# Performance work log

Measured on AMD Instinct MI355X. Metric: run time of the kernel, lower is better.

The kernel has to match this reference:

```python
import jax, jax.numpy as jnp
import numpy as np

HEADS = 16

def setup_inputs() -> dict:
    key = jax.random.key(0)
    ks = jax.random.split(key, 8)
    N, S, E = 4, 2048, 1024
    D = E // HEADS
    values = jax.random.normal(ks[0], (N, S, E), jnp.float32)
    keys_t = jax.random.normal(ks[1], (N, S, E), jnp.float32)
    query = jax.random.normal(ks[2], (N, S, E), jnp.float32)
    mask = jnp.ones((N, 1, 1, S), jnp.float32)  # broadcasts vs (N,H,Q,K)
    # keras Dense(head_dim, use_bias=False) on last-dim head_dim input: kernel (D, D)
    Wv = jax.random.normal(ks[3], (D, D), jnp.float32) * 0.05
    Wk = jax.random.normal(ks[4], (D, D), jnp.float32) * 0.05
    Wq = jax.random.normal(ks[5], (D, D), jnp.float32) * 0.05
    Wo = jax.random.normal(ks[6], (E, E), jnp.float32) * 0.02
    bo = jnp.zeros((E,), jnp.float32)
    return {"values": values, "keys": keys_t, "query": query, "mask": mask,
            "Wv": Wv, "Wk": Wk, "Wq": Wq, "Wo": Wo, "bo": bo}

def reference(values, keys, query, mask, Wv, Wk, Wq, Wo, bo):
    N, S, E = values.shape
    H = HEADS
    D = E // H
    # reshape to (N, len, H, D), then per-head shared Dense(D) projections
    v = values.reshape(N, S, H, D) @ Wv
    k = keys.reshape(N, S, H, D) @ Wk
    q = query.reshape(N, query.shape[1], H, D) @ Wq
    energy = jnp.einsum('nqhd,nkhd->nhqk', q, k)  # (N,H,Q,K)
    energy = jnp.where(mask == 0, jnp.float32(-1e20), energy)
    # NOTE: scaled by sqrt(embed_size), matching the original module
    attn = jax.nn.softmax(energy / jnp.sqrt(jnp.float32(E)), axis=3)
    out = jnp.einsum('nhql,nlhd->nqhd', attn, v)  # (N,Q,H,D)
    out = out.reshape(N, q.shape[1], E)
    return out @ Wo + bo
```

## Files before the change

### kernel.cpp

```cpp
#include <hip/hip_runtime.h>


typedef unsigned short u16;
typedef __attribute__((ext_vector_type(8))) short s16x8;
typedef __attribute__((ext_vector_type(8))) unsigned short u16x8;
typedef __attribute__((ext_vector_type(4))) float f32x4;
typedef __attribute__((ext_vector_type(4))) unsigned int u32x4;

#define GLL16(gsrc, ldst)                                                     \
    __builtin_amdgcn_global_load_lds(                                         \
        (const __attribute__((address_space(1))) void*)(gsrc),                \
        (__attribute__((address_space(3))) void*)(ldst), 16, 0, 0)

static __device__ __forceinline__ u16 f2bf(float f) {
    unsigned u = __builtin_bit_cast(unsigned, f);
    unsigned r = u + 0x7FFFu + ((u >> 16) & 1u);
    return (u16)(r >> 16);
}

__global__ __launch_bounds__(256) void prep_wot_k(const float* __restrict__ Wo,
                                                  u16* __restrict__ WoT) {
    __shared__ float tl[64][68];
    const int k0 = blockIdx.x * 64, n0 = blockIdx.y * 64;
    const int rr = threadIdx.x >> 2;
    const int c4 = (threadIdx.x & 3) * 16;
#pragma unroll
    for (int j = 0; j < 4; ++j)
        *(f32x4*)(&tl[rr][c4 + j * 4]) =
            *(const f32x4*)(Wo + (size_t)(k0 + rr) * 1024 + n0 + c4 + j * 4);
    __syncthreads();
    unsigned pk[8];
#pragma unroll
    for (int j = 0; j < 8; ++j)
        pk[j] = (unsigned)f2bf(tl[c4 + 2 * j][rr]) |
                ((unsigned)f2bf(tl[c4 + 2 * j + 1][rr]) << 16);
    u16* dst = WoT + (size_t)(n0 + rr) * 1024 + k0 + c4;
    *(u32x4*)(dst)     = u32x4{pk[0], pk[1], pk[2], pk[3]};
    *(u32x4*)(dst + 8) = u32x4{pk[4], pk[5], pk[6], pk[7]};
}

__global__ __launch_bounds__(256) void proj3(
    const float* __restrict__ xv, const float* __restrict__ xk,
    const float* __restrict__ xq, const float* __restrict__ Wv,
    const float* __restrict__ Wk, const float* __restrict__ Wq,
    u16* __restrict__ vout, u16* __restrict__ kout, u16* __restrict__ qout) {
    __shared__ float Xs[64][68];
    __shared__ float Ws[64][64];
    const int tid = threadIdx.x;
    const int rr = tid >> 2;
    const int c4 = (tid & 3) * 16;
    const int t0 = blockIdx.x * 64;
    const int h = blockIdx.y;
    const int n = t0 >> 11;
    const int srow = t0 & 2047;

    const float* X[3] = {xv, xk, xq};
    const float* W[3] = {Wv, Wk, Wq};
    u16* O[3] = {vout, kout, qout};

#pragma unroll
    for (int tz = 0; tz < 3; ++tz) {
#pragma unroll
        for (int j = 0; j < 4; ++j) {
            *(f32x4*)(&Ws[rr][c4 + j * 4]) =
                *(const f32x4*)(W[tz] + rr * 64 + c4 + j * 4);
            *(f32x4*)(&Xs[rr][c4 + j * 4]) = *(const f32x4*)(
                X[tz] + (size_t)(t0 + rr) * 1024 + h * 64 + c4 + j * 4);
        }
        __syncthreads();
        float acc[16];
#pragma unroll
        for (int j = 0; j < 16; ++j) acc[j] = 0.f;
#pragma unroll 4
        for (int k = 0; k < 64; ++k) {
            float xval = Xs[rr][k];
#pragma unroll
            for (int j = 0; j < 16; ++j) acc[j] += xval * Ws[k][c4 + j];
        }
        unsigned pk[8];
#pragma unroll
        for (int j = 0; j < 8; ++j)
            pk[j] = (unsigned)f2bf(acc[2 * j]) |
                    ((unsigned)f2bf(acc[2 * j + 1]) << 16);
        u16* dst =
            O[tz] + ((size_t)(n * 16 + h) * 2048 + srow + rr) * 64 + c4;
        *(u32x4*)(dst)     = u32x4{pk[0], pk[1], pk[2], pk[3]};
        *(u32x4*)(dst + 8) = u32x4{pk[4], pk[5], pk[6], pk[7]};
        __syncthreads();
    }
}

__global__ __launch_bounds__(256, 2) void attn_fused(
    const u16* __restrict__ qb, const u16* __restrict__ kb,
    const u16* __restrict__ vb, const float* __restrict__ mask,
    u16* __restrict__ ob) {
    __shared__ char Kl[2][8192];
    __shared__ char Vt[2][8192];
    __shared__ char Pl[4][4096];

    const int tid = threadIdx.x;
    const int w = tid >> 6;
    const int l = tid & 63;
    const int g = l >> 4;
    const int lr = l & 15;
    const int nh = blockIdx.y;
    const int n = nh >> 4, h = nh & 15;
    const int q0 = blockIdx.x * 128 + w * 32;

    const u16* Qg = qb + (size_t)nh * (2048 * 64);
    const u16* Kg = kb + (size_t)nh * (2048 * 64);
    const u16* Vg = vb + (size_t)nh * (2048 * 64);

    s16x8 aq[2][2];
#pragma unroll
    for (int mt = 0; mt < 2; ++mt)
#pragma unroll
        for (int ks = 0; ks < 2; ++ks)
            aq[mt][ks] = *(const s16x8*)(Qg +
                (size_t)(q0 + mt * 16 + lr) * 64 + ks * 32 + g * 8);

    f32x4 oacc[2][4];
    float mrow[2][4], lpart[2][4];
#pragma unroll
    for (int mt = 0; mt < 2; ++mt) {
#pragma unroll
        for (int r = 0; r < 4; ++r) { mrow[mt][r] = -1e30f; lpart[mt][r] = 0.f; }
#pragma unroll
        for (int nd = 0; nd < 4; ++nd) oacc[mt][nd] = f32x4{0.f, 0.f, 0.f, 0.f};
    }

    u32x4 vreg[2];
#pragma unroll
    for (int i = 0; i < 2; ++i) {
        int j = w * 2 + i;
        int kk = j * 8 + (l >> 3);
        int c = (l & 7) ^ (kk & 7);
        GLL16(Kg + (size_t)kk * 64 + c * 8, &Kl[0][j * 1024]);
    }
#pragma unroll
    for (int it = 0; it < 2; ++it) {
        int kk = it * 32 + (tid >> 3);
        int dc = tid & 7;
        vreg[it] = *(const u32x4*)(Vg + (size_t)kk * 64 + dc * 8);
    }
#pragma unroll
    for (int it = 0; it < 2; ++it) {
        int kk = it * 32 + (tid >> 3);
        int dc = tid & 7;
        u16x8 vv = __builtin_bit_cast(u16x8, vreg[it]);
#pragma unroll
        for (int jj = 0; jj < 8; ++jj) {
            int d = dc * 8 + jj;
            *(u16*)(&Vt[0][d * 128 + ((kk * 2) ^ ((jj ^ dc) << 4))]) = vv[jj];
        }
    }
    __syncthreads();

    for (int t = 0; t < 32; ++t) {
        const int buf = t & 1;
        const int kv0 = t * 64;
        if (t < 31) {
#pragma unroll
            for (int i = 0; i < 2; ++i) {
                int j = w * 2 + i;
                int kk = j * 8 + (l >> 3);
                int c = (l & 7) ^ (kk & 7);
                GLL16(Kg + (size_t)(kv0 + 64 + kk) * 64 + c * 8,
                      &Kl[buf ^ 1][j * 1024]);
            }
#pragma unroll
            for (int it = 0; it < 2; ++it) {
                int kk = it * 32 + (tid >> 3);
                int dc = tid & 7;
                vreg[it] = *(const u32x4*)(Vg + (size_t)(kv0 + 64 + kk) * 64 + dc * 8);
            }
        }

        f32x4 sacc[2][4];
#pragma unroll
        for (int mt = 0; mt < 2; ++mt)
#pragma unroll
            for (int nt = 0; nt < 4; ++nt) sacc[mt][nt] = f32x4{0.f, 0.f, 0.f, 0.f};
#pragma unroll
        for (int ks = 0; ks < 2; ++ks) {
            s16x8 bk[4];
#pragma unroll
            for (int nt = 0; nt < 4; ++nt) {
                int krow = nt * 16 + lr;
                int c = (ks * 4 + g) ^ (krow & 7);
                bk[nt] = *(const s16x8*)(&Kl[buf][krow * 128 + c * 16]);
            }
#pragma unroll
            for (int mt = 0; mt < 2; ++mt)
#pragma unroll
                for (int nt = 0; nt < 4; ++nt)
                    sacc[mt][nt] = __builtin_amdgcn_mfma_f32_16x16x32_bf16(
                        aq[mt][ks], bk[nt], sacc[mt][nt], 0, 0, 0);
        }

        float mv[4];
#pragma unroll
        for (int nt = 0; nt < 4; ++nt)
            mv[nt] = mask[(size_t)n * 2048 + kv0 + nt * 16 + lr];

#pragma unroll
        for (int mt = 0; mt < 2; ++mt) {
            float lg[4][4];
#pragma unroll
            for (int nt = 0; nt < 4; ++nt)
#pragma unroll
                for (int r = 0; r < 4; ++r)
                    lg[r][nt] = (mv[nt] != 0.f) ? sacc[mt][nt][r] * 0.03125f
                                                : (-1e20f * 0.03125f);
#pragma unroll
            for (int r = 0; r < 4; ++r) {
                float rm = fmaxf(fmaxf(lg[r][0], lg[r][1]),
                                 fmaxf(lg[r][2], lg[r][3]));
#pragma unroll
                for (int off = 1; off < 16; off <<= 1)
                    rm = fmaxf(rm, __shfl_xor(rm, off, 64));
                float mold = mrow[mt][r];
                float mnew = fmaxf(mold, rm);
                mrow[mt][r] = mnew;
                float corr = __expf(mold - mnew);
                float ps = 0.f;
#pragma unroll
                for (int nt = 0; nt < 4; ++nt) {
                    float p = __expf(lg[r][nt] - mnew);
                    lg[r][nt] = p;
                    ps += p;
                }
                lpart[mt][r] = lpart[mt][r] * corr + ps;
#pragma unroll
                for (int nd = 0; nd < 4; ++nd) oacc[mt][nd][r] *= corr;
            }
#pragma unroll
            for (int r = 0; r < 4; ++r) {
                int qh = mt * 16 + g * 4 + r;
#pragma unroll
                for (int nt = 0; nt < 4; ++nt) {
                    int kh = nt * 16 + lr;
                    *(u16*)(&Pl[w][qh * 128 + ((kh * 2) ^ ((qh & 7) << 4))]) =
                        f2bf(lg[r][nt]);
                }
            }
        }

#pragma unroll
        for (int ks2 = 0; ks2 < 2; ++ks2) {
            s16x8 ap[2], bv[4];
#pragma unroll
            for (int mt = 0; mt < 2; ++mt) {
                int qh = mt * 16 + lr;
                ap[mt] = *(const s16x8*)(&Pl[w][qh * 128 +
                             ((ks2 * 64 + g * 16) ^ ((qh & 7) << 4))]);
            }
#pragma unroll
            for (int nd = 0; nd < 4; ++nd) {
                int d = nd * 16 + lr;
                int sw = ((d & 7) ^ ((d >> 3) & 7)) << 4;
                bv[nd] = *(const s16x8*)(&Vt[buf][d * 128 +
                             ((ks2 * 64 + g * 16) ^ sw)]);
            }
#pragma unroll
            for (int mt = 0; mt < 2; ++mt)
#pragma unroll
                for (int nd = 0; nd < 4; ++nd)
                    oacc[mt][nd] = __builtin_amdgcn_mfma_f32_16x16x32_bf16(
                        ap[mt], bv[nd], oacc[mt][nd], 0, 0, 0);
        }

        if (t < 31) {
#pragma unroll
            for (int it = 0; it < 2; ++it) {
                int kk = it * 32 + (tid >> 3);
                int dc = tid & 7;
                u16x8 vv = __builtin_bit_cast(u16x8, vreg[it]);
#pragma unroll
                for (int jj = 0; jj < 8; ++jj) {
                    int d = dc * 8 + jj;
                    *(u16*)(&Vt[buf ^ 1][d * 128 + ((kk * 2) ^ ((jj ^ dc) << 4))]) = vv[jj];
                }
            }
        }
        __syncthreads();
    }

#pragma unroll
    for (int mt = 0; mt < 2; ++mt)
#pragma unroll
        for (int r = 0; r < 4; ++r) {
            float s = lpart[mt][r];
#pragma unroll
            for (int off = 1; off < 16; off <<= 1) s += __shfl_xor(s, off, 64);
            float inv = 1.0f / s;
            int q = q0 + mt * 16 + g * 4 + r;
            size_t obase = ((size_t)n * 2048 + q) * 1024 + h * 64;
#pragma unroll
            for (int nd = 0; nd < 4; ++nd)
                ob[obase + nd * 16 + lr] = f2bf(oacc[mt][nd][r] * inv);
        }
}

__global__ __launch_bounds__(256, 2) void ogemm(const u16* __restrict__ A,
                                                const u16* __restrict__ B,
                                                const float* __restrict__ bias,
                                                float* __restrict__ C) {
    __shared__ char Al[2][8192];
    __shared__ char Bl[2][8192];
    const int tid = threadIdx.x;
    const int w = tid >> 6, l = tid & 63, g = l >> 4, lr = l & 15;
    const int m0 = blockIdx.x * 128, n0 = blockIdx.y * 128;
    const int wr = w >> 1, wc = w & 1;

    f32x4 acc[4][4];
#pragma unroll
    for (int mt = 0; mt < 4; ++mt)
#pragma unroll
        for (int nt = 0; nt < 4; ++nt) acc[mt][nt] = f32x4{0.f, 0.f, 0.f, 0.f};

    auto stage = [&](int bufi, int kt) {
#pragma unroll
        for (int i = 0; i < 2; ++i) {
            int j = w * 2 + i;
            int rrow = j * 16 + (l >> 2);
            int c = l & 3;
            GLL16(A + (size_t)(m0 + rrow) * 1024 + kt * 32 + c * 8,
                  &Al[bufi][j * 1024]);
            GLL16(B + (size_t)(n0 + rrow) * 1024 + kt * 32 + c * 8,
                  &Bl[bufi][j * 1024]);
        }
    };
    stage(0, 0);
    __syncthreads();
    for (int kt = 0; kt < 32; ++kt) {
        const int buf = kt & 1;
        if (kt < 31) stage(buf ^ 1, kt + 1);
        s16x8 a[4], b[4];
#pragma unroll
        for (int mt = 0; mt < 4; ++mt)
            a[mt] = *(const s16x8*)(&Al[buf][(wr * 64 + mt * 16 + lr) * 64 + g * 16]);
#pragma unroll
        for (int nt = 0; nt < 4; ++nt)
            b[nt] = *(const s16x8*)(&Bl[buf][(wc * 64 + nt * 16 + lr) * 64 + g * 16]);
#pragma unroll
        for (int mt = 0; mt < 4; ++mt)
#pragma unroll
            for (int nt = 0; nt < 4; ++nt)
                acc[mt][nt] = __builtin_amdgcn_mfma_f32_16x16x32_bf16(
                    a[mt], b[nt], acc[mt][nt], 0, 0, 0);
        __syncthreads();
    }
#pragma unroll
    for (int nt = 0; nt < 4; ++nt) {
        int ncol = n0 + wc * 64 + nt * 16 + lr;
        float bv = bias[ncol];
#pragma unroll
        for (int mt = 0; mt < 4; ++mt)
#pragma unroll
            for (int r = 0; r < 4; ++r) {
                int m = m0 + wr * 64 + mt * 16 + g * 4 + r;
                C[(size_t)m * 1024 + ncol] = acc[mt][nt][r] + bv;
            }
    }
}

extern "C" void kernel_launch(void* const* d_in, const int* in_sizes, int n_in,
                              void* d_out, int out_size, void* d_ws,
                              size_t ws_size, hipStream_t stream) {
    const float* values = (const float*)d_in[0];
    const float* keys   = (const float*)d_in[1];
    const float* query  = (const float*)d_in[2];
    const float* mask   = (const float*)d_in[3];
    const float* Wv     = (const float*)d_in[4];
    const float* Wk     = (const float*)d_in[5];
    const float* Wq     = (const float*)d_in[6];
    const float* Wo     = (const float*)d_in[7];
    const float* bo     = (const float*)d_in[8];
    float* out = (float*)d_out;

    char* ws = (char*)d_ws;
    const size_t SZ = 16777216;
    u16* qbf = (u16*)(ws + 0 * SZ);
    u16* kbf = (u16*)(ws + 1 * SZ);
    u16* vbf = (u16*)(ws + 2 * SZ);
    u16* obf = (u16*)(ws + 3 * SZ);
    u16* wot = (u16*)(ws + 4 * SZ);

    prep_wot_k<<<dim3(16, 16), dim3(256), 0, stream>>>(Wo, wot);
    proj3<<<dim3(128, 16), dim3(256), 0, stream>>>(values, keys, query, Wv, Wk,
                                                   Wq, vbf, kbf, qbf);
    attn_fused<<<dim3(16, 64), dim3(256), 0, stream>>>(qbf, kbf, vbf, mask, obf);
    ogemm<<<dim3(64, 8), dim3(256), 0, stream>>>(obf, wot, bo, out);
}
```

Measured before the change: 410.3 us.

## Use MFMA for QKV projections and streamline attention softmax with lazy rescaling

```diff
diff --git a/kernel.cpp b/kernel.cpp
--- a/kernel.cpp
+++ b/kernel.cpp
@@ -12,10 +12,19 @@
         (const __attribute__((address_space(1))) void*)(gsrc),                \
         (__attribute__((address_space(3))) void*)(ldst), 16, 0, 0)
 
+#if __has_builtin(__builtin_amdgcn_exp2f)
+#define EXP2(x) __builtin_amdgcn_exp2f(x)
+#else
+#define EXP2(x) exp2f(x)
+#endif
+
 static __device__ __forceinline__ u16 f2bf(float f) {
     unsigned u = __builtin_bit_cast(unsigned, f);
     unsigned r = u + 0x7FFFu + ((u >> 16) & 1u);
     return (u16)(r >> 16);
+}
+static __device__ __forceinline__ u16 f2bf_fast(float f) {
+    return (u16)((__builtin_bit_cast(unsigned, f) + 0x8000u) >> 16);
 }
 
 __global__ __launch_bounds__(256) void prep_wot_k(const float* __restrict__ Wo,
@@ -39,54 +48,94 @@
     *(u32x4*)(dst + 8) = u32x4{pk[4], pk[5], pk[6], pk[7]};
 }
 
-__global__ __launch_bounds__(256) void proj3(
+__global__ __launch_bounds__(256) void prep_wt3(const float* __restrict__ Wv,
+                                                const float* __restrict__ Wk,
+                                                const float* __restrict__ Wq,
+                                                u16* __restrict__ wt) {
+    __shared__ float tl[64][65];
+    const float* W = blockIdx.x == 0 ? Wv : (blockIdx.x == 1 ? Wk : Wq);
+    u16* dst = wt + blockIdx.x * 4096;
+    const int r = threadIdx.x >> 2;
+    const int c = (threadIdx.x & 3) * 16;
+#pragma unroll
+    for (int j = 0; j < 4; ++j)
+        *(f32x4*)(&tl[r][c + j * 4]) = *(const f32x4*)(W + r * 64 + c + j * 4);
+    __syncthreads();
+    unsigned pk[8];
+#pragma unroll
+    for (int j = 0; j < 8; ++j)
+        pk[j] = (unsigned)f2bf(tl[c + 2 * j][r]) |
+                ((unsigned)f2bf(tl[c + 2 * j + 1][r]) << 16);
+    u16* d = dst + r * 64 + c;
+    *(u32x4*)(d)     = u32x4{pk[0], pk[1], pk[2], pk[3]};
+    *(u32x4*)(d + 8) = u32x4{pk[4], pk[5], pk[6], pk[7]};
+}
+
+__global__ __launch_bounds__(256) void proj3_mfma(
     const float* __restrict__ xv, const float* __restrict__ xk,
-    const float* __restrict__ xq, const float* __restrict__ Wv,
-    const float* __restrict__ Wk, const float* __restrict__ Wq,
+    const float* __restrict__ xq, const u16* __restrict__ wt3,
     u16* __restrict__ vout, u16* __restrict__ kout, u16* __restrict__ qout) {
-    __shared__ float Xs[64][68];
-    __shared__ float Ws[64][64];
     const int tid = threadIdx.x;
-    const int rr = tid >> 2;
-    const int c4 = (tid & 3) * 16;
-    const int t0 = blockIdx.x * 64;
+    const int w = tid >> 6, l = tid & 63, g = l >> 4, lr = l & 15;
+    const int t0 = blockIdx.x * 128;
     const int h = blockIdx.y;
     const int n = t0 >> 11;
     const int srow = t0 & 2047;
+    const int r0 = w * 32;
 
     const float* X[3] = {xv, xk, xq};
-    const float* W[3] = {Wv, Wk, Wq};
     u16* O[3] = {vout, kout, qout};
 
 #pragma unroll
     for (int tz = 0; tz < 3; ++tz) {
-#pragma unroll
-        for (int j = 0; j < 4; ++j) {
-            *(f32x4*)(&Ws[rr][c4 + j * 4]) =
-                *(const f32x4*)(W[tz] + rr * 64 + c4 + j * 4);
-            *(f32x4*)(&Xs[rr][c4 + j * 4]) = *(const f32x4*)(
-                X[tz] + (size_t)(t0 + rr) * 1024 + h * 64 + c4 + j * 4);
-        }
-        __syncthreads();
-        float acc[16];
-#pragma unroll
-        for (int j = 0; j < 16; ++j) acc[j] = 0.f;
-#pragma unroll 4
-        for (int k = 0; k < 64; ++k) {
-            float xval = Xs[rr][k];
-#pragma unroll
-            for (int j = 0; j < 16; ++j) acc[j] += xval * Ws[k][c4 + j];
-        }
-        unsigned pk[8];
-#pragma unroll
-        for (int j = 0; j < 8; ++j)
-            pk[j] = (unsigned)f2bf(acc[2 * j]) |
-                    ((unsigned)f2bf(acc[2 * j + 1]) << 16);
-        u16* dst =
-            O[tz] + ((size_t)(n * 16 + h) * 2048 + srow + rr) * 64 + c4;
-        *(u32x4*)(dst)     = u32x4{pk[0], pk[1], pk[2], pk[3]};
-        *(u32x4*)(dst + 8) = u32x4{pk[4], pk[5], pk[6], pk[7]};
-        __syncthreads();
+        const u16* WT = wt3 + tz * 4096;
+        s16x8 bw[2][4];
+#pragma unroll
+        for (int ks = 0; ks < 2; ++ks)
+#pragma unroll
+            for (int nd = 0; nd < 4; ++nd)
+                bw[ks][nd] = *(const s16x8*)(WT + (nd * 16 + lr) * 64 +
+                                             ks * 32 + g * 8);
+        s16x8 ax[2][2];
+#pragma unroll
+        for (int mt = 0; mt < 2; ++mt)
+#pragma unroll
+            for (int ks = 0; ks < 2; ++ks) {
+                const float* src = X[tz] +
+                    (size_t)(t0 + r0 + mt * 16 + lr) * 1024 + h * 64 +
+                    ks * 32 + g * 8;
+                f32x4 x0 = *(const f32x4*)(src);
+                f32x4 x1 = *(const f32x4*)(src + 4);
+                union { s16x8 v; u16 e[8]; } u;
+#pragma unroll
+                for (int j = 0; j < 4; ++j) {
+                    u.e[j]     = f2bf(x0[j]);
+                    u.e[4 + j] = f2bf(x1[j]);
+                }
+                ax[mt][ks] = u.v;
+            }
+        f32x4 acc[2][4];
+#pragma unroll
+        for (int mt = 0; mt < 2; ++mt)
+#pragma unroll
+            for (int nd = 0; nd < 4; ++nd) acc[mt][nd] = f32x4{0.f, 0.f, 0.f, 0.f};
+#pragma unroll
+        for (int ks = 0; ks < 2; ++ks)
+#pragma unroll
+            for (int mt = 0; mt < 2; ++mt)
+#pragma unroll
+                for (int nd = 0; nd < 4; ++nd)
+                    acc[mt][nd] = __builtin_amdgcn_mfma_f32_16x16x32_bf16(
+                        ax[mt][ks], bw[ks][nd], acc[mt][nd], 0, 0, 0);
+        u16* Ob = O[tz] + ((size_t)(n * 16 + h) * 2048 + srow + r0) * 64;
+#pragma unroll
+        for (int mt = 0; mt < 2; ++mt)
+#pragma unroll
+            for (int nd = 0; nd < 4; ++nd)
+#pragma unroll
+                for (int r = 0; r < 4; ++r)
+                    Ob[(size_t)(mt * 16 + g * 4 + r) * 64 + nd * 16 + lr] =
+                        f2bf(acc[mt][nd][r]);
     }
 }
 
@@ -103,14 +152,23 @@
     const int l = tid & 63;
     const int g = l >> 4;
     const int lr = l & 15;
-    const int nh = blockIdx.y;
+    const int bid = blockIdx.x;
+    const int swz = (bid & 7) * 128 + (bid >> 3);
+    const int nh = swz >> 4;
+    const int qt = swz & 15;
     const int n = nh >> 4, h = nh & 15;
-    const int q0 = blockIdx.x * 128 + w * 32;
+    const int q0 = qt * 128 + w * 32;
 
     const u16* Qg = qb + (size_t)nh * (2048 * 64);
     const u16* Kg = kb + (size_t)nh * (2048 * 64);
     const u16* Vg = vb + (size_t)nh * (2048 * 64);
 
+    const float CSC = 0.04508422f;
+    const float THR = 8.0f;
+    const short one_bf = (short)0x3F80;
+    const s16x8 vones = {one_bf, one_bf, one_bf, one_bf,
+                         one_bf, one_bf, one_bf, one_bf};
+
     s16x8 aq[2][2];
 #pragma unroll
     for (int mt = 0; mt < 2; ++mt)
@@ -120,11 +178,14 @@
                 (size_t)(q0 + mt * 16 + lr) * 64 + ks * 32 + g * 8);
 
     f32x4 oacc[2][4];
-    float mrow[2][4], lpart[2][4];
+    f32x4 osum[2];
+    float mrow[2][4];
+    float wmin = -1e30f;
 #pragma unroll
     for (int mt = 0; mt < 2; ++mt) {
-#pragma unroll
-        for (int r = 0; r < 4; ++r) { mrow[mt][r] = -1e30f; lpart[mt][r] = 0.f; }
+        osum[mt] = f32x4{0.f, 0.f, 0.f, 0.f};
+#pragma unroll
+        for (int r = 0; r < 4; ++r) mrow[mt][r] = -1e30f;
 #pragma unroll
         for (int nd = 0; nd < 4; ++nd) oacc[mt][nd] = f32x4{0.f, 0.f, 0.f, 0.f};
     }
@@ -159,6 +220,12 @@
     for (int t = 0; t < 32; ++t) {
         const int buf = t & 1;
         const int kv0 = t * 64;
+
+        float mv[4];
+#pragma unroll
+        for (int nt = 0; nt < 4; ++nt)
+            mv[nt] = mask[(size_t)n * 2048 + kv0 + nt * 16 + lr];
+
         if (t < 31) {
 #pragma unroll
             for (int i = 0; i < 2; ++i) {
@@ -198,53 +265,71 @@
                         aq[mt][ks], bk[nt], sacc[mt][nt], 0, 0, 0);
         }
 
-        float mv[4];
+        float mb[4];
 #pragma unroll
         for (int nt = 0; nt < 4; ++nt)
-            mv[nt] = mask[(size_t)n * 2048 + kv0 + nt * 16 + lr];
-
-#pragma unroll
-        for (int mt = 0; mt < 2; ++mt) {
-            float lg[4][4];
+            mb[nt] = (mv[nt] != 0.f) ? 0.f : -1e30f;
+
+        float lg[2][4][4];
+#pragma unroll
+        for (int mt = 0; mt < 2; ++mt)
 #pragma unroll
             for (int nt = 0; nt < 4; ++nt)
 #pragma unroll
                 for (int r = 0; r < 4; ++r)
-                    lg[r][nt] = (mv[nt] != 0.f) ? sacc[mt][nt][r] * 0.03125f
-                                                : (-1e20f * 0.03125f);
-#pragma unroll
-            for (int r = 0; r < 4; ++r) {
-                float rm = fmaxf(fmaxf(lg[r][0], lg[r][1]),
-                                 fmaxf(lg[r][2], lg[r][3]));
-#pragma unroll
-                for (int off = 1; off < 16; off <<= 1)
-                    rm = fmaxf(rm, __shfl_xor(rm, off, 64));
-                float mold = mrow[mt][r];
-                float mnew = fmaxf(mold, rm);
-                mrow[mt][r] = mnew;
-                float corr = __expf(mold - mnew);
-                float ps = 0.f;
-#pragma unroll
-                for (int nt = 0; nt < 4; ++nt) {
-                    float p = __expf(lg[r][nt] - mnew);
-                    lg[r][nt] = p;
-                    ps += p;
+                    lg[mt][r][nt] = fmaf(sacc[mt][nt][r], CSC, mb[nt]);
+
+        float tmax = lg[0][0][0];
+#pragma unroll
+        for (int mt = 0; mt < 2; ++mt)
+#pragma unroll
+            for (int r = 0; r < 4; ++r)
+#pragma unroll
+                for (int nt = 0; nt < 4; ++nt)
+                    tmax = fmaxf(tmax, lg[mt][r][nt]);
+
+        if (!__all(tmax <= wmin + THR)) {
+#pragma unroll
+            for (int mt = 0; mt < 2; ++mt)
+#pragma unroll
+                for (int r = 0; r < 4; ++r) {
+                    float rm = fmaxf(fmaxf(lg[mt][r][0], lg[mt][r][1]),
+                                     fmaxf(lg[mt][r][2], lg[mt][r][3]));
+#pragma unroll
+                    for (int off = 1; off < 16; off <<= 1)
+                        rm = fmaxf(rm, __shfl_xor(rm, off, 64));
+                    float mold = mrow[mt][r];
+                    float mnew = fmaxf(mold, rm);
+                    float corr = EXP2(mold - mnew);
+                    mrow[mt][r] = mnew;
+                    osum[mt][r] *= corr;
+#pragma unroll
+                    for (int nd = 0; nd < 4; ++nd) oacc[mt][nd][r] *= corr;
                 }
-                lpart[mt][r] = lpart[mt][r] * corr + ps;
-#pragma unroll
-                for (int nd = 0; nd < 4; ++nd) oacc[mt][nd][r] *= corr;
-            }
+            float lmin = mrow[0][0];
+#pragma unroll
+            for (int mt = 0; mt < 2; ++mt)
+#pragma unroll
+                for (int r = 0; r < 4; ++r) lmin = fminf(lmin, mrow[mt][r]);
+            lmin = fminf(lmin, __shfl_xor(lmin, 16, 64));
+            lmin = fminf(lmin, __shfl_xor(lmin, 32, 64));
+            wmin = lmin;
+        }
+
+#pragma unroll
+        for (int mt = 0; mt < 2; ++mt)
 #pragma unroll
             for (int r = 0; r < 4; ++r) {
                 int qh = mt * 16 + g * 4 + r;
+                float m = mrow[mt][r];
 #pragma unroll
                 for (int nt = 0; nt < 4; ++nt) {
+                    float p = EXP2(lg[mt][r][nt] - m);
                     int kh = nt * 16 + lr;
                     *(u16*)(&Pl[w][qh * 128 + ((kh * 2) ^ ((qh & 7) << 4))]) =
-                        f2bf(lg[r][nt]);
+                        f2bf_fast(p);
                 }
             }
-        }
 
 #pragma unroll
         for (int ks2 = 0; ks2 < 2; ++ks2) {
@@ -263,11 +348,14 @@
                              ((ks2 * 64 + g * 16) ^ sw)]);
             }
 #pragma unroll
-            for (int mt = 0; mt < 2; ++mt)
+            for (int mt = 0; mt < 2; ++mt) {
+                osum[mt] = __builtin_amdgcn_mfma_f32_16x16x32_bf16(
+                    ap[mt], vones, osum[mt], 0, 0, 0);
 #pragma unroll
                 for (int nd = 0; nd < 4; ++nd)
                     oacc[mt][nd] = __builtin_amdgcn_mfma_f32_16x16x32_bf16(
                         ap[mt], bv[nd], oacc[mt][nd], 0, 0, 0);
+            }
         }
 
         if (t < 31) {
@@ -290,10 +378,7 @@
     for (int mt = 0; mt < 2; ++mt)
 #pragma unroll
         for (int r = 0; r < 4; ++r) {
-            float s = lpart[mt][r];
-#pragma unroll
-            for (int off = 1; off < 16; off <<= 1) s += __shfl_xor(s, off, 64);
-            float inv = 1.0f / s;
+            float inv = 1.0f / osum[mt][r];
             int q = q0 + mt * 16 + g * 4 + r;
             size_t obase = ((size_t)n * 2048 + q) * 1024 + h * 64;
 #pragma unroll
@@ -386,10 +471,12 @@
     u16* vbf = (u16*)(ws + 2 * SZ);
     u16* obf = (u16*)(ws + 3 * SZ);
     u16* wot = (u16*)(ws + 4 * SZ);
+    u16* wt3 = (u16*)(ws + 4 * SZ + 2097152);
 
     prep_wot_k<<<dim3(16, 16), dim3(256), 0, stream>>>(Wo, wot);
-    proj3<<<dim3(128, 16), dim3(256), 0, stream>>>(values, keys, query, Wv, Wk,
-                                                   Wq, vbf, kbf, qbf);
-    attn_fused<<<dim3(16, 64), dim3(256), 0, stream>>>(qbf, kbf, vbf, mask, obf);
+    prep_wt3<<<dim3(3), dim3(256), 0, stream>>>(Wv, Wk, Wq, wt3);
+    proj3_mfma<<<dim3(64, 16), dim3(256), 0, stream>>>(values, keys, query,
+                                                       wt3, vbf, kbf, qbf);
+    attn_fused<<<dim3(1024), dim3(256), 0, stream>>>(qbf, kbf, vbf, mask, obf);
     ogemm<<<dim3(64, 8), dim3(256), 0, stream>>>(obf, wot, bo, out);
 }
```

Result: faster. 357.2 us (-12.9%).
